# Kernel tuning notes

Hardware: AMD Instinct MI355X
Metric: run time of the kernel (lower is better)

## Reference

```python
import jax, jax.numpy as jnp
import numpy as np

GFD = 4096   # global feature dim (VGG fc7)
DH = 1024    # 2 * hidden_dim


def setup_inputs() -> dict:
    key = jax.random.key(0)
    ks = jax.random.split(key, 10)
    b, t_k = 32, 196
    s = lambda fan_in: 1.0 / np.sqrt(fan_in)
    return {
        "global_features": jax.random.normal(ks[0], (b, t_k, GFD), jnp.float32),
        "s_t_hat": jax.random.normal(ks[1], (b, DH), jnp.float32),
        "coverage_img": jnp.zeros((b, t_k, 1), jnp.float32),
        # params
        "Wg": jax.random.normal(ks[2], (GFD, GFD), jnp.float32) * s(GFD),
        "bg": jnp.zeros((GFD,), jnp.float32),
        "Gs": jax.random.normal(ks[3], (GFD, DH), jnp.float32) * s(GFD),
        "bgs": jnp.zeros((DH,), jnp.float32),
        "Wgs": jax.random.normal(ks[4], (DH, DH), jnp.float32) * s(DH),  # w_g_star, no bias
        "Wdec": jax.random.normal(ks[5], (DH, DH), jnp.float32) * s(DH),  # decode_proj
        "bdec": jnp.zeros((DH,), jnp.float32),
        "v": jax.random.normal(ks[6], (DH, 1), jnp.float32) * s(DH),  # score vector, no bias
    }


def reference(global_features, s_t_hat, coverage_img, Wg, bg, Gs, bgs, Wgs, Wdec, bdec, v):
    # g_star: project 4096-d region features -> 1024-d   [b, t_k, DH]
    g1 = global_features @ Wg + bg
    g_star = g1 @ Gs + bgs
    # additive (Bahdanau) scores with coverage
    w_g_star = g_star @ Wgs                       # [b, t_k, DH]
    dec_fea = s_t_hat @ Wdec + bdec               # [b, DH]
    e_a = jnp.tanh(w_g_star + dec_fea[:, None, :] + coverage_img)  # [b, t_k, DH]
    scores = e_a @ v                              # [b, t_k, 1]
    alpha_a = jax.nn.softmax(scores, axis=1)      # softmax over regions
    # attention-weighted context (the bmm)
    c_img = jnp.einsum("bt,btd->bd", alpha_a[..., 0], g_star)  # [b, DH]
    coverage_new = coverage_img + alpha_a
    return c_img, coverage_new, alpha_a
```

## Files before the change

kernel.cpp:

```cpp
#include <hip/hip_runtime.h>
#include <hip/hip_bf16.h>

typedef __attribute__((ext_vector_type(8))) short short8;
typedef __attribute__((ext_vector_type(4))) float floatx4;

#define GLOBAL_AS __attribute__((address_space(1)))
#define LDS_AS    __attribute__((address_space(3)))

__device__ __forceinline__ unsigned short f2bf_rne(float x) {
  unsigned int u = __float_as_uint(x);
  u += 0x7fffu + ((u >> 16) & 1u);
  return (unsigned short)(u >> 16);
}

__global__ void cast_f32_bf16_kernel(const float* __restrict__ in,
                                     unsigned short* __restrict__ out, int n8) {
  int i = blockIdx.x * 256 + threadIdx.x;
  if (i >= n8) return;
  const float4* p = (const float4*)in;
  float4 v0 = p[2 * i], v1 = p[2 * i + 1];
  short8 o;
  o[0] = (short)f2bf_rne(v0.x); o[1] = (short)f2bf_rne(v0.y);
  o[2] = (short)f2bf_rne(v0.z); o[3] = (short)f2bf_rne(v0.w);
  o[4] = (short)f2bf_rne(v1.x); o[5] = (short)f2bf_rne(v1.y);
  o[6] = (short)f2bf_rne(v1.z); o[7] = (short)f2bf_rne(v1.w);
  *(short8*)(out + 8 * (size_t)i) = o;
}

__global__ void transpose_cast_kernel(const float* __restrict__ in,
                                      unsigned short* __restrict__ out, int R, int C) {
  __shared__ unsigned short tile[32][33];
  int tx = threadIdx.x & 31, ty = threadIdx.x >> 5;
  int r0 = blockIdx.y * 32, c0 = blockIdx.x * 32;
#pragma unroll
  for (int j = 0; j < 32; j += 8)
    tile[ty + j][tx] = f2bf_rne(in[(size_t)(r0 + ty + j) * C + c0 + tx]);
  __syncthreads();
#pragma unroll
  for (int j = 0; j < 32; j += 8)
    out[(size_t)(c0 + ty + j) * R + r0 + tx] = tile[tx][ty + j];
}

__global__ void init_vec_kernel(const float* __restrict__ src, float* __restrict__ dst) {
  int i = blockIdx.x * 256 + threadIdx.x;
  dst[i] = src[i];
}
__global__ void bias1_accum_kernel(const float* __restrict__ bg, const float* __restrict__ Gs,
                                   float* __restrict__ bias1) {
  int j = blockIdx.x * 256 + threadIdx.x;
  int k0 = blockIdx.y * 256;
  float acc = 0.f;
  for (int k = 0; k < 256; ++k) acc += bg[k0 + k] * Gs[(size_t)(k0 + k) * 1024 + j];
  atomicAdd(&bias1[j], acc);
}

__global__ void init_dec_kernel(const float* __restrict__ bdec, float* __restrict__ dec) {
  int i = blockIdx.x * 256 + threadIdx.x;
  dec[i] = bdec[i & 1023];
}
__global__ void dec_accum_kernel(const float* __restrict__ sth, const float* __restrict__ Wdec,
                                 float* __restrict__ dec) {
  __shared__ float ss[32][128];
  const int tid = threadIdx.x;
  const int k0 = blockIdx.y * 128;
  for (int i = tid; i < 32 * 128; i += 256) {
    int bb = i >> 7, kk = i & 127;
    ss[bb][kk] = sth[bb * 1024 + k0 + kk];
  }
  __syncthreads();
  const int j = blockIdx.x * 256 + tid;
  float acc[32];
#pragma unroll
  for (int b = 0; b < 32; ++b) acc[b] = 0.f;
  for (int kk = 0; kk < 128; ++kk) {
    float w = Wdec[(size_t)(k0 + kk) * 1024 + j];
#pragma unroll
    for (int b = 0; b < 32; ++b) acc[b] += ss[b][kk] * w;
  }
  for (int b = 0; b < 32; ++b) atomicAdd(&dec[b * 1024 + j], acc[b]);
}

template <bool HAS_BIAS>
__global__ __launch_bounds__(256, 2) void gemm_bt_kernel(
    const unsigned short* __restrict__ A, const unsigned short* __restrict__ BT,
    const float* __restrict__ bias, float* __restrict__ C, int M, int N, int K) {
  __shared__ unsigned short lds_a[128 * 32];
  __shared__ unsigned short lds_b[128 * 32];
  const int tid = threadIdx.x;
  const int lane = tid & 63;
  const int wave = tid >> 6;
  const int wm = wave >> 1, wn = wave & 1;
  const int quad = lane >> 4, col = lane & 15;
  const int m0 = blockIdx.y * 128, n0 = blockIdx.x * 128;

  floatx4 acc[4][4] = {};

  const int srow = tid >> 2;
  const int skoff = (tid & 3) * 8;
  const unsigned short* a_ptr = A + (size_t)(m0 + srow) * K + skoff;
  const unsigned short* b_ptr = BT + (size_t)(n0 + srow) * K + skoff;
  const size_t rowskip = (size_t)64 * K;
  char* la_dst = (char*)lds_a + tid * 16;
  char* lb_dst = (char*)lds_b + tid * 16;

  for (int kt = 0; kt < K; kt += 32) {
    __syncthreads();
    __builtin_amdgcn_global_load_lds((const GLOBAL_AS void*)(a_ptr), (LDS_AS void*)(la_dst), 16, 0, 0);
    __builtin_amdgcn_global_load_lds((const GLOBAL_AS void*)(a_ptr + rowskip), (LDS_AS void*)(la_dst + 4096), 16, 0, 0);
    __builtin_amdgcn_global_load_lds((const GLOBAL_AS void*)(b_ptr), (LDS_AS void*)(lb_dst), 16, 0, 0);
    __builtin_amdgcn_global_load_lds((const GLOBAL_AS void*)(b_ptr + rowskip), (LDS_AS void*)(lb_dst + 4096), 16, 0, 0);
    a_ptr += 32; b_ptr += 32;
    __syncthreads();
    short8 af[4], bf[4];
#pragma unroll
    for (int t = 0; t < 4; ++t) {
      af[t] = *(const short8*)((const char*)lds_a + (wm * 64 + t * 16 + col) * 64 + quad * 16);
      bf[t] = *(const short8*)((const char*)lds_b + (wn * 64 + t * 16 + col) * 64 + quad * 16);
    }
#pragma unroll
    for (int tm = 0; tm < 4; ++tm)
#pragma unroll
      for (int tn = 0; tn < 4; ++tn)
        acc[tm][tn] = __builtin_amdgcn_mfma_f32_16x16x32_bf16(af[tm], bf[tn], acc[tm][tn], 0, 0, 0);
  }

#pragma unroll
  for (int tm = 0; tm < 4; ++tm) {
    const int mg = m0 + wm * 64 + tm * 16 + quad * 4;
#pragma unroll
    for (int tn = 0; tn < 4; ++tn) {
      const int ng = n0 + wn * 64 + tn * 16 + col;
      const float bv = HAS_BIAS ? bias[ng] : 0.0f;
#pragma unroll
      for (int r = 0; r < 4; ++r)
        C[(size_t)(mg + r) * N + ng] = acc[tm][tn][r] + bv;
    }
  }
}

__global__ void scores_kernel(const float* __restrict__ w, const float* __restrict__ dec,
                              const float* __restrict__ cov, const float* __restrict__ v,
                              float* __restrict__ scores) {
  const int row = blockIdx.x * 4 + (threadIdx.x >> 6);
  const int lane = threadIdx.x & 63;
  const int b = row / 196;
  const float cv = cov[row];
  const float* wr = w + (size_t)row * 1024;
  const float* dr = dec + b * 1024;
  float acc = 0.f;
#pragma unroll
  for (int i = 0; i < 4; ++i) {
    int d = i * 256 + lane * 4;
    float4 wv = *(const float4*)(wr + d);
    float4 dv = *(const float4*)(dr + d);
    float4 vv = *(const float4*)(v + d);
    acc += tanhf(wv.x + dv.x + cv) * vv.x;
    acc += tanhf(wv.y + dv.y + cv) * vv.y;
    acc += tanhf(wv.z + dv.z + cv) * vv.z;
    acc += tanhf(wv.w + dv.w + cv) * vv.w;
  }
  for (int off = 32; off > 0; off >>= 1) acc += __shfl_down(acc, off, 64);
  if (lane == 0) scores[row] = acc;
}

__global__ void softmax_ctx_kernel(const float* __restrict__ scores,
                                   const float* __restrict__ gstar,
                                   const float* __restrict__ cov, float* __restrict__ out) {
  const int b = blockIdx.x, tid = threadIdx.x;
  const int lane = tid & 63, wid = tid >> 6;
  __shared__ float sal[256];
  __shared__ float red[8];
  float s = (tid < 196) ? scores[b * 196 + tid] : -1e30f;
  float m = s;
  for (int off = 32; off > 0; off >>= 1) m = fmaxf(m, __shfl_xor(m, off, 64));
  if (lane == 0) red[wid] = m;
  __syncthreads();
  m = fmaxf(fmaxf(red[0], red[1]), fmaxf(red[2], red[3]));
  float e = (tid < 196) ? __expf(s - m) : 0.f;
  float t = e;
  for (int off = 32; off > 0; off >>= 1) t += __shfl_xor(t, off, 64);
  if (lane == 0) red[4 + wid] = t;
  __syncthreads();
  const float tot = red[4] + red[5] + red[6] + red[7];
  const float a = e / tot;
  sal[tid] = a;
  if (tid < 196) {
    out[32768 + b * 196 + tid] = cov[b * 196 + tid] + a;
    out[32768 + 6272 + b * 196 + tid] = a;
  }
  __syncthreads();
  const float* gs = gstar + (size_t)b * 196 * 1024 + tid * 4;
  float4 acc = make_float4(0.f, 0.f, 0.f, 0.f);
  for (int t2 = 0; t2 < 196; ++t2) {
    float a2 = sal[t2];
    float4 g = *(const float4*)(gs + (size_t)t2 * 1024);
    acc.x += a2 * g.x; acc.y += a2 * g.y; acc.z += a2 * g.z; acc.w += a2 * g.w;
  }
  *(float4*)(out + b * 1024 + tid * 4) = acc;
}

extern "C" void kernel_launch(void* const* d_in, const int* in_sizes, int n_in,
                              void* d_out, int out_size, void* d_ws, size_t ws_size,
                              hipStream_t stream) {
  (void)in_sizes; (void)n_in; (void)out_size; (void)ws_size;
  const float* gf   = (const float*)d_in[0];
  const float* sth  = (const float*)d_in[1];
  const float* cov  = (const float*)d_in[2];
  const float* Wg   = (const float*)d_in[3];
  const float* bg   = (const float*)d_in[4];
  const float* Gs   = (const float*)d_in[5];
  const float* bgs  = (const float*)d_in[6];
  const float* Wgs  = (const float*)d_in[7];
  const float* Wdec = (const float*)d_in[8];
  const float* bdec = (const float*)d_in[9];
  const float* v    = (const float*)d_in[10];
  float* out = (float*)d_out;

  char* ws = (char*)d_ws;
  unsigned short* gf_bf  = (unsigned short*)(ws + 0);
  float*          w_f    = (float*)(ws + 0);
  unsigned short* Wg_bf  = (unsigned short*)(ws + 51380224);
  float*          gstar_f = (float*)(ws + 51380224);
  unsigned short* GsT    = (unsigned short*)(ws + 84934656);
  unsigned short* WgsT   = (unsigned short*)(ws + 84934656);
  float*          C1T_f  = (float*)(ws + 93323264);
  unsigned short* gstar_b = (unsigned short*)(ws + 93323264);
  unsigned short* C1T_b  = (unsigned short*)(ws + 110100480);
  float*          bias1  = (float*)(ws + 118489088);
  float*          dec    = (float*)(ws + 118493184);
  float*          scores = (float*)(ws + 118624256);

  cast_f32_bf16_kernel<<<12544, 256, 0, stream>>>(gf, gf_bf, 3211264);
  cast_f32_bf16_kernel<<<8192, 256, 0, stream>>>(Wg, Wg_bf, 2097152);
  transpose_cast_kernel<<<dim3(32, 128), 256, 0, stream>>>(Gs, GsT, 4096, 1024);
  init_vec_kernel<<<4, 256, 0, stream>>>(bgs, bias1);
  bias1_accum_kernel<<<dim3(4, 16), 256, 0, stream>>>(bg, Gs, bias1);
  gemm_bt_kernel<false><<<dim3(32, 8), 256, 0, stream>>>(GsT, Wg_bf, nullptr, C1T_f, 1024, 4096, 4096);
  cast_f32_bf16_kernel<<<2048, 256, 0, stream>>>(C1T_f, C1T_b, 524288);
  transpose_cast_kernel<<<dim3(32, 32), 256, 0, stream>>>(Wgs, WgsT, 1024, 1024);
  init_dec_kernel<<<128, 256, 0, stream>>>(bdec, dec);
  dec_accum_kernel<<<dim3(4, 8), 256, 0, stream>>>(sth, Wdec, dec);
  gemm_bt_kernel<true><<<dim3(8, 49), 256, 0, stream>>>(gf_bf, C1T_b, bias1, gstar_f, 6272, 1024, 4096);
  cast_f32_bf16_kernel<<<3136, 256, 0, stream>>>(gstar_f, gstar_b, 802816);
  gemm_bt_kernel<false><<<dim3(8, 49), 256, 0, stream>>>(gstar_b, WgsT, nullptr, w_f, 6272, 1024, 1024);
  scores_kernel<<<1568, 256, 0, stream>>>(w_f, dec, cov, v, scores);
  softmax_ctx_kernel<<<32, 256, 0, stream>>>(scores, gstar_f, cov, out);
}
```

Before: 545.9 us.

## Split-K GEMMs with atomics, fuse score epilogue into GEMM, parallelize context

The two large GEMMs now use split-K across blockIdx.z with atomicAdd accumulation into pre-zeroed or bias-broadcast outputs, so more blocks fill the GPU. The third GEMM computes the tanh/v-dot score reduction in its epilogue, removing the fp32 w_g_star write and the separate scores pass. The softmax and context bmm are split, and the context is spread over 256 blocks instead of 32. The cost is extra zeroing and broadcast passes, atomic traffic, and nondeterministic summation order.

```diff
diff --git a/kernel.cpp b/kernel.cpp
--- a/kernel.cpp
+++ b/kernel.cpp
@@ -41,9 +41,17 @@
     out[(size_t)(c0 + ty + j) * R + r0 + tx] = tile[tx][ty + j];
 }
 
+__global__ void zero4_kernel(float* __restrict__ p, int n4) {
+  int i = blockIdx.x * 256 + threadIdx.x;
+  if (i < n4) ((float4*)p)[i] = make_float4(0.f, 0.f, 0.f, 0.f);
+}
 __global__ void init_vec_kernel(const float* __restrict__ src, float* __restrict__ dst) {
   int i = blockIdx.x * 256 + threadIdx.x;
   dst[i] = src[i];
+}
+__global__ void bcast_bias_kernel(const float* __restrict__ bias1, float* __restrict__ dst) {
+  int i = blockIdx.x * 256 + threadIdx.x;
+  ((float4*)dst)[i] = ((const float4*)bias1)[i & 255];
 }
 __global__ void bias1_accum_kernel(const float* __restrict__ bg, const float* __restrict__ Gs,
                                    float* __restrict__ bias1) {
@@ -80,10 +88,67 @@
   for (int b = 0; b < 32; ++b) atomicAdd(&dec[b * 1024 + j], acc[b]);
 }
 
-template <bool HAS_BIAS>
-__global__ __launch_bounds__(256, 2) void gemm_bt_kernel(
+__global__ __launch_bounds__(256, 4) void gemm_bt_atomic_kernel(
     const unsigned short* __restrict__ A, const unsigned short* __restrict__ BT,
-    const float* __restrict__ bias, float* __restrict__ C, int M, int N, int K) {
+    float* __restrict__ C, int M, int N, int K, int kchunk) {
+  __shared__ unsigned short lds_a[128 * 32];
+  __shared__ unsigned short lds_b[128 * 32];
+  const int tid = threadIdx.x;
+  const int lane = tid & 63;
+  const int wave = tid >> 6;
+  const int wm = wave >> 1, wn = wave & 1;
+  const int quad = lane >> 4, col = lane & 15;
+  const int m0 = blockIdx.y * 128, n0 = blockIdx.x * 128;
+  const int kbase = blockIdx.z * kchunk;
+
+  floatx4 acc[4][4] = {};
+
+  const int srow = tid >> 2;
+  const int skoff = (tid & 3) * 8;
+  const unsigned short* a_ptr = A + (size_t)(m0 + srow) * K + kbase + skoff;
+  const unsigned short* b_ptr = BT + (size_t)(n0 + srow) * K + kbase + skoff;
+  const size_t rowskip = (size_t)64 * K;
+  char* la_dst = (char*)lds_a + tid * 16;
+  char* lb_dst = (char*)lds_b + tid * 16;
+
+  for (int kt = 0; kt < kchunk; kt += 32) {
+    __syncthreads();
+    __builtin_amdgcn_global_load_lds((const GLOBAL_AS void*)(a_ptr), (LDS_AS void*)(la_dst), 16, 0, 0);
+    __builtin_amdgcn_global_load_lds((const GLOBAL_AS void*)(a_ptr + rowskip), (LDS_AS void*)(la_dst + 4096), 16, 0, 0);
+    __builtin_amdgcn_global_load_lds((const GLOBAL_AS void*)(b_ptr), (LDS_AS void*)(lb_dst), 16, 0, 0);
+    __builtin_amdgcn_global_load_lds((const GLOBAL_AS void*)(b_ptr + rowskip), (LDS_AS void*)(lb_dst + 4096), 16, 0, 0);
+    a_ptr += 32; b_ptr += 32;
+    __syncthreads();
+    short8 af[4], bf[4];
+#pragma unroll
+    for (int t = 0; t < 4; ++t) {
+      af[t] = *(const short8*)((const char*)lds_a + (wm * 64 + t * 16 + col) * 64 + quad * 16);
+      bf[t] = *(const short8*)((const char*)lds_b + (wn * 64 + t * 16 + col) * 64 + quad * 16);
+    }
+#pragma unroll
+    for (int tm = 0; tm < 4; ++tm)
+#pragma unroll
+      for (int tn = 0; tn < 4; ++tn)
+        acc[tm][tn] = __builtin_amdgcn_mfma_f32_16x16x32_bf16(af[tm], bf[tn], acc[tm][tn], 0, 0, 0);
+  }
+
+#pragma unroll
+  for (int tm = 0; tm < 4; ++tm) {
+    const int mg = m0 + wm * 64 + tm * 16 + quad * 4;
+#pragma unroll
+    for (int tn = 0; tn < 4; ++tn) {
+      const int ng = n0 + wn * 64 + tn * 16 + col;
+#pragma unroll
+      for (int r = 0; r < 4; ++r)
+        atomicAdd(&C[(size_t)(mg + r) * N + ng], acc[tm][tn][r]);
+    }
+  }
+}
+
+__global__ __launch_bounds__(256, 2) void gemm_scores_kernel(
+    const unsigned short* __restrict__ A, const unsigned short* __restrict__ BT,
+    const float* __restrict__ dec, const float* __restrict__ cov,
+    const float* __restrict__ v, float* __restrict__ scores, int M, int N, int K) {
   __shared__ unsigned short lds_a[128 * 32];
   __shared__ unsigned short lds_b[128 * 32];
   const int tid = threadIdx.x;
@@ -124,51 +189,35 @@
         acc[tm][tn] = __builtin_amdgcn_mfma_f32_16x16x32_bf16(af[tm], bf[tn], acc[tm][tn], 0, 0, 0);
   }
 
+  const int n_base = n0 + wn * 64;
+  float vv[4];
+#pragma unroll
+  for (int tn = 0; tn < 4; ++tn) vv[tn] = v[n_base + tn * 16 + col];
 #pragma unroll
   for (int tm = 0; tm < 4; ++tm) {
-    const int mg = m0 + wm * 64 + tm * 16 + quad * 4;
-#pragma unroll
-    for (int tn = 0; tn < 4; ++tn) {
-      const int ng = n0 + wn * 64 + tn * 16 + col;
-      const float bv = HAS_BIAS ? bias[ng] : 0.0f;
-#pragma unroll
-      for (int r = 0; r < 4; ++r)
-        C[(size_t)(mg + r) * N + ng] = acc[tm][tn][r] + bv;
+#pragma unroll
+    for (int r = 0; r < 4; ++r) {
+      const int row = m0 + wm * 64 + tm * 16 + quad * 4 + r;
+      const int b = row / 196;
+      const float cw = cov[row];
+      const float* dr = dec + b * 1024 + n_base;
+      float s = 0.f;
+#pragma unroll
+      for (int tn = 0; tn < 4; ++tn)
+        s += tanhf(acc[tm][tn][r] + dr[tn * 16 + col] + cw) * vv[tn];
+      s += __shfl_xor(s, 1, 64);
+      s += __shfl_xor(s, 2, 64);
+      s += __shfl_xor(s, 4, 64);
+      s += __shfl_xor(s, 8, 64);
+      if ((lane & 15) == 0) atomicAdd(&scores[row], s);
     }
   }
 }
 
-__global__ void scores_kernel(const float* __restrict__ w, const float* __restrict__ dec,
-                              const float* __restrict__ cov, const float* __restrict__ v,
-                              float* __restrict__ scores) {
-  const int row = blockIdx.x * 4 + (threadIdx.x >> 6);
-  const int lane = threadIdx.x & 63;
-  const int b = row / 196;
-  const float cv = cov[row];
-  const float* wr = w + (size_t)row * 1024;
-  const float* dr = dec + b * 1024;
-  float acc = 0.f;
-#pragma unroll
-  for (int i = 0; i < 4; ++i) {
-    int d = i * 256 + lane * 4;
-    float4 wv = *(const float4*)(wr + d);
-    float4 dv = *(const float4*)(dr + d);
-    float4 vv = *(const float4*)(v + d);
-    acc += tanhf(wv.x + dv.x + cv) * vv.x;
-    acc += tanhf(wv.y + dv.y + cv) * vv.y;
-    acc += tanhf(wv.z + dv.z + cv) * vv.z;
-    acc += tanhf(wv.w + dv.w + cv) * vv.w;
-  }
-  for (int off = 32; off > 0; off >>= 1) acc += __shfl_down(acc, off, 64);
-  if (lane == 0) scores[row] = acc;
-}
-
-__global__ void softmax_ctx_kernel(const float* __restrict__ scores,
-                                   const float* __restrict__ gstar,
-                                   const float* __restrict__ cov, float* __restrict__ out) {
+__global__ void softmax_kernel(const float* __restrict__ scores, const float* __restrict__ cov,
+                               float* __restrict__ alpha_ws, float* __restrict__ out) {
   const int b = blockIdx.x, tid = threadIdx.x;
   const int lane = tid & 63, wid = tid >> 6;
-  __shared__ float sal[256];
   __shared__ float red[8];
   float s = (tid < 196) ? scores[b * 196 + tid] : -1e30f;
   float m = s;
@@ -183,20 +232,30 @@
   __syncthreads();
   const float tot = red[4] + red[5] + red[6] + red[7];
   const float a = e / tot;
-  sal[tid] = a;
   if (tid < 196) {
+    alpha_ws[b * 196 + tid] = a;
     out[32768 + b * 196 + tid] = cov[b * 196 + tid] + a;
     out[32768 + 6272 + b * 196 + tid] = a;
   }
-  __syncthreads();
-  const float* gs = gstar + (size_t)b * 196 * 1024 + tid * 4;
-  float4 acc = make_float4(0.f, 0.f, 0.f, 0.f);
-  for (int t2 = 0; t2 < 196; ++t2) {
-    float a2 = sal[t2];
-    float4 g = *(const float4*)(gs + (size_t)t2 * 1024);
-    acc.x += a2 * g.x; acc.y += a2 * g.y; acc.z += a2 * g.z; acc.w += a2 * g.w;
-  }
-  *(float4*)(out + b * 1024 + tid * 4) = acc;
+}
+
+__global__ __launch_bounds__(256) void ctx_kernel(const float* __restrict__ alpha,
+                                                  const float* __restrict__ gstar,
+                                                  float* __restrict__ out) {
+  const int b = blockIdx.y;
+  const int colbase = blockIdx.x * 128;
+  const int c = threadIdx.x & 127;
+  const int half = threadIdx.x >> 7;
+  const float* g = gstar + ((size_t)b * 196 + half * 98) * 1024 + colbase + c;
+  const float* al = alpha + b * 196 + half * 98;
+  float acc = 0.f;
+#pragma unroll 7
+  for (int t = 0; t < 98; ++t) acc += al[t] * g[(size_t)t * 1024];
+  __shared__ float part[256];
+  part[threadIdx.x] = acc;
+  __syncthreads();
+  if (threadIdx.x < 128)
+    out[b * 1024 + colbase + threadIdx.x] = part[threadIdx.x] + part[threadIdx.x + 128];
 }
 
 extern "C" void kernel_launch(void* const* d_in, const int* in_sizes, int n_in,
@@ -217,32 +276,35 @@
   float* out = (float*)d_out;
 
   char* ws = (char*)d_ws;
-  unsigned short* gf_bf  = (unsigned short*)(ws + 0);
-  float*          w_f    = (float*)(ws + 0);
-  unsigned short* Wg_bf  = (unsigned short*)(ws + 51380224);
+  unsigned short* gf_bf   = (unsigned short*)(ws + 0);
+  float*          alpha   = (float*)(ws + 0);
+  unsigned short* Wg_bf   = (unsigned short*)(ws + 51380224);
   float*          gstar_f = (float*)(ws + 51380224);
-  unsigned short* GsT    = (unsigned short*)(ws + 84934656);
-  unsigned short* WgsT   = (unsigned short*)(ws + 84934656);
-  float*          C1T_f  = (float*)(ws + 93323264);
+  unsigned short* GsT     = (unsigned short*)(ws + 84934656);
+  unsigned short* WgsT    = (unsigned short*)(ws + 84934656);
+  float*          C1T_f   = (float*)(ws + 93323264);
   unsigned short* gstar_b = (unsigned short*)(ws + 93323264);
-  unsigned short* C1T_b  = (unsigned short*)(ws + 110100480);
-  float*          bias1  = (float*)(ws + 118489088);
-  float*          dec    = (float*)(ws + 118493184);
-  float*          scores = (float*)(ws + 118624256);
+  unsigned short* C1T_b   = (unsigned short*)(ws + 110100480);
+  float*          bias1   = (float*)(ws + 118489088);
+  float*          dec     = (float*)(ws + 118493184);
+  float*          scores  = (float*)(ws + 118624256);
 
   cast_f32_bf16_kernel<<<12544, 256, 0, stream>>>(gf, gf_bf, 3211264);
   cast_f32_bf16_kernel<<<8192, 256, 0, stream>>>(Wg, Wg_bf, 2097152);
   transpose_cast_kernel<<<dim3(32, 128), 256, 0, stream>>>(Gs, GsT, 4096, 1024);
   init_vec_kernel<<<4, 256, 0, stream>>>(bgs, bias1);
   bias1_accum_kernel<<<dim3(4, 16), 256, 0, stream>>>(bg, Gs, bias1);
-  gemm_bt_kernel<false><<<dim3(32, 8), 256, 0, stream>>>(GsT, Wg_bf, nullptr, C1T_f, 1024, 4096, 4096);
+  zero4_kernel<<<4096, 256, 0, stream>>>(C1T_f, 1048576);
+  gemm_bt_atomic_kernel<<<dim3(32, 8, 4), 256, 0, stream>>>(GsT, Wg_bf, C1T_f, 1024, 4096, 4096, 1024);
   cast_f32_bf16_kernel<<<2048, 256, 0, stream>>>(C1T_f, C1T_b, 524288);
   transpose_cast_kernel<<<dim3(32, 32), 256, 0, stream>>>(Wgs, WgsT, 1024, 1024);
   init_dec_kernel<<<128, 256, 0, stream>>>(bdec, dec);
   dec_accum_kernel<<<dim3(4, 8), 256, 0, stream>>>(sth, Wdec, dec);
-  gemm_bt_kernel<true><<<dim3(8, 49), 256, 0, stream>>>(gf_bf, C1T_b, bias1, gstar_f, 6272, 1024, 4096);
+  bcast_bias_kernel<<<6272, 256, 0, stream>>>(bias1, gstar_f);
+  gemm_bt_atomic_kernel<<<dim3(8, 49, 2), 256, 0, stream>>>(gf_bf, C1T_b, gstar_f, 6272, 1024, 4096, 2048);
   cast_f32_bf16_kernel<<<3136, 256, 0, stream>>>(gstar_f, gstar_b, 802816);
-  gemm_bt_kernel<false><<<dim3(8, 49), 256, 0, stream>>>(gstar_b, WgsT, nullptr, w_f, 6272, 1024, 1024);
-  scores_kernel<<<1568, 256, 0, stream>>>(w_f, dec, cov, v, scores);
-  softmax_ctx_kernel<<<32, 256, 0, stream>>>(scores, gstar_f, cov, out);
-}
+  zero4_kernel<<<7, 256, 0, stream>>>(scores, 1568);
+  gemm_scores_kernel<<<dim3(8, 49), 256, 0, stream>>>(gstar_b, WgsT, dec, cov, v, scores, 6272, 1024, 1024);
+  softmax_kernel<<<32, 256, 0, stream>>>(scores, cov, alpha, out);
+  ctx_kernel<<<dim3(8, 32), 256, 0, stream>>>(alpha, gstar_f, out);
+}
```

Result: slower. 572.4 us (+4.8%).
